# Optimization experiments

Measured on AMD Instinct MI355X. Metric: run time of the kernel, lower is better.

## Reference

```python
import jax, jax.numpy as jnp
import numpy as np

N_NODES = 50000
N_EDGES = 1600000
D_EDGE = 64
D_VERT = 64
D_IN = D_EDGE + 2 * D_VERT  # 192
D_HID = 128
D_OUT = 64


def setup_inputs() -> dict:
    key = jax.random.key(0)
    ks = jax.random.split(key, 8)
    edata = jax.random.normal(ks[0], (N_EDGES, D_EDGE), dtype=jnp.float32)
    vfeat = jax.random.normal(ks[1], (N_NODES, D_VERT), dtype=jnp.float32)
    W1 = jax.random.normal(ks[2], (D_IN, D_HID), dtype=jnp.float32) * (1.0 / np.sqrt(D_IN))
    b1 = jnp.zeros((D_HID,), dtype=jnp.float32)
    W2 = jax.random.normal(ks[3], (D_HID, D_OUT), dtype=jnp.float32) * (1.0 / np.sqrt(D_HID))
    b2 = jnp.zeros((D_OUT,), dtype=jnp.float32)
    senders = jax.random.randint(ks[4], (N_EDGES,), 0, N_NODES, dtype=jnp.int64)
    receivers = jax.random.randint(ks[5], (N_EDGES,), 0, N_NODES, dtype=jnp.int64)
    return {"edata": edata, "vfeat": vfeat, "W1": W1, "b1": b1,
            "W2": W2, "b2": b2, "senders": senders, "receivers": receivers}


def reference(edata, vfeat, W1, b1, W2, b2, senders, receivers):
    # Per-edge gather of receiver/sender vertex features, concat with edge
    # features (matches torch.cat([edata[e], v[recv], v[send]]) per edge,
    # vectorized), then updater MLP: Linear -> ReLU -> Linear.
    x = jnp.concatenate([edata, vfeat[receivers], vfeat[senders]], axis=-1)  # [E, 192]
    h = jax.nn.relu(x @ W1 + b1)  # [E, 128]
    return h @ W2 + b2            # [E, 64]
```

## Files before the change

### kernel.cpp

```cpp
#include <hip/hip_runtime.h>
#include <hip/hip_bf16.h>

#define E_TOTAL   1600000
#define NV        50000
#define DE        64
#define DV        64
#define DIN       192
#define DHID      128
#define DOUT      64
#define TILE_M    64
#define XS        200
#define HS        136
#define NTILES    (E_TOTAL / TILE_M)

typedef __bf16 bf16x8  __attribute__((ext_vector_type(8)));
typedef __bf16 bf16x4  __attribute__((ext_vector_type(4)));
typedef float  floatx4 __attribute__((ext_vector_type(4)));
typedef float  fx4     __attribute__((ext_vector_type(4)));

static __device__ __forceinline__ unsigned short f2bf(float f) {
    unsigned int u = __float_as_uint(f);
    u += 0x7fffu + ((u >> 16) & 1u);
    return (unsigned short)(u >> 16);
}

__global__ void prep_kernel(const float* __restrict__ W1, const float* __restrict__ W2,
                            const float* __restrict__ vfeat,
                            unsigned short* __restrict__ w1t,
                            unsigned short* __restrict__ w2t,
                            unsigned short* __restrict__ vfb, int do_vfb) {
    int tid = blockIdx.x * blockDim.x + threadIdx.x;
    int stride = gridDim.x * blockDim.x;
    for (int i = tid; i < DIN * DHID; i += stride) {
        int n = i / DIN, k = i % DIN;
        w1t[i] = f2bf(W1[k * DHID + n]);
    }
    for (int i = tid; i < DHID * DOUT; i += stride) {
        int n = i / DHID, k = i % DHID;
        w2t[i] = f2bf(W2[k * DOUT + n]);
    }
    if (do_vfb) {
        const fx4* src = (const fx4*)vfeat;
        ushort4* dst = (ushort4*)vfb;
        int n4 = NV * DV / 4;
        for (int i = tid; i < n4; i += stride) {
            fx4 v = src[i];
            ushort4 o;
            o.x = f2bf(v[0]); o.y = f2bf(v[1]); o.z = f2bf(v[2]); o.w = f2bf(v[3]);
            dst[i] = o;
        }
    }
}

template <bool USE_VFB>
__global__ __launch_bounds__(256, 2) void edge_mlp(
    const float* __restrict__ edata,
    const float* __restrict__ vfeat,
    const float* __restrict__ b1,
    const float* __restrict__ b2,
    const int* __restrict__ senders,
    const int* __restrict__ receivers,
    const unsigned short* __restrict__ w1t,
    const unsigned short* __restrict__ w2t,
    const unsigned short* __restrict__ vfb,
    float* __restrict__ out) {
    __shared__ unsigned short xb[TILE_M * XS];
    __shared__ unsigned short hb[TILE_M * HS];

    const int tid  = threadIdx.x;
    const int lane = tid & 63;
    const int wave = tid >> 6;
    const int l15  = lane & 15;
    const int quad = lane >> 4;

    bf16x8 w1f[6][2];
    bf16x8 w2f[4];
    {
        for (int nb = 0; nb < 2; ++nb) {
            int n = wave * 32 + nb * 16 + l15;
            const unsigned short* p = w1t + n * DIN + quad * 8;
            for (int ks = 0; ks < 6; ++ks)
                w1f[ks][nb] = *(const bf16x8*)(p + ks * 32);
        }
        int n2 = wave * 16 + l15;
        const unsigned short* p2 = w2t + n2 * DHID + quad * 8;
        for (int ks = 0; ks < 4; ++ks)
            w2f[ks] = *(const bf16x8*)(p2 + ks * 32);
    }
    float b1v[2][4], b2v[4];
#pragma unroll
    for (int nb = 0; nb < 2; ++nb)
#pragma unroll
        for (int r = 0; r < 4; ++r)
            b1v[nb][r] = b1[wave * 32 + nb * 16 + quad * 4 + r];
#pragma unroll
    for (int r = 0; r < 4; ++r)
        b2v[r] = b2[wave * 16 + quad * 4 + r];

    for (int t = blockIdx.x; t < NTILES; t += gridDim.x) {
        const long e0 = (long)t * TILE_M;

        {
#pragma unroll
            for (int it = 0; it < 4; ++it) {
                int idx = it * 256 + tid;
                int e = idx >> 4;
                int c = idx & 15;
                fx4 v = __builtin_nontemporal_load((const fx4*)(edata + (e0 + e) * DE + c * 4));
                bf16x4 o;
                o[0] = (__bf16)v[0]; o[1] = (__bf16)v[1];
                o[2] = (__bf16)v[2]; o[3] = (__bf16)v[3];
                *(bf16x4*)(xb + e * XS + c * 4) = o;
            }
            if constexpr (USE_VFB) {
#pragma unroll
                for (int it = 0; it < 4; ++it) {
                    int idx = it * 256 + tid;
                    int e = idx >> 4;
                    int g = (idx >> 3) & 1;
                    int c = idx & 7;
                    int row = g ? senders[e0 + e] : receivers[e0 + e];
                    uint4 v = *(const uint4*)(vfb + row * DV + c * 8);
                    *(uint4*)(xb + e * XS + DE + g * DV + c * 8) = v;
                }
            } else {
#pragma unroll
                for (int it = 0; it < 8; ++it) {
                    int idx = it * 256 + tid;
                    int e = idx >> 5;
                    int g = (idx >> 4) & 1;
                    int c = idx & 15;
                    int row = g ? senders[e0 + e] : receivers[e0 + e];
                    fx4 v = *(const fx4*)(vfeat + (long)row * DV + c * 4);
                    bf16x4 o;
                    o[0] = (__bf16)v[0]; o[1] = (__bf16)v[1];
                    o[2] = (__bf16)v[2]; o[3] = (__bf16)v[3];
                    *(bf16x4*)(xb + e * XS + DE + g * DV + c * 4) = o;
                }
            }
        }
        __syncthreads();

        floatx4 acc[4][2];
#pragma unroll
        for (int mb = 0; mb < 4; ++mb)
#pragma unroll
            for (int nb = 0; nb < 2; ++nb)
                acc[mb][nb] = (floatx4){b1v[nb][0], b1v[nb][1], b1v[nb][2], b1v[nb][3]};
#pragma unroll
        for (int ks = 0; ks < 6; ++ks) {
            bf16x8 a[4];
#pragma unroll
            for (int mb = 0; mb < 4; ++mb)
                a[mb] = *(const bf16x8*)(xb + (mb * 16 + l15) * XS + ks * 32 + quad * 8);
#pragma unroll
            for (int mb = 0; mb < 4; ++mb)
#pragma unroll
                for (int nb = 0; nb < 2; ++nb)
                    acc[mb][nb] = __builtin_amdgcn_mfma_f32_16x16x32_bf16(
                        w1f[ks][nb], a[mb], acc[mb][nb], 0, 0, 0);
        }

#pragma unroll
        for (int mb = 0; mb < 4; ++mb)
#pragma unroll
            for (int nb = 0; nb < 2; ++nb) {
                bf16x4 o;
#pragma unroll
                for (int r = 0; r < 4; ++r) {
                    float v = acc[mb][nb][r];
                    o[r] = (__bf16)(v > 0.f ? v : 0.f);
                }
                *(bf16x4*)(hb + (mb * 16 + l15) * HS + wave * 32 + nb * 16 + quad * 4) = o;
            }
        __syncthreads();

        floatx4 acc2[4];
#pragma unroll
        for (int mb = 0; mb < 4; ++mb)
            acc2[mb] = (floatx4){b2v[0], b2v[1], b2v[2], b2v[3]};
#pragma unroll
        for (int ks = 0; ks < 4; ++ks)
#pragma unroll
            for (int mb = 0; mb < 4; ++mb) {
                bf16x8 a2 = *(const bf16x8*)(hb + (mb * 16 + l15) * HS + ks * 32 + quad * 8);
                acc2[mb] = __builtin_amdgcn_mfma_f32_16x16x32_bf16(w2f[ks], a2, acc2[mb], 0, 0, 0);
            }

#pragma unroll
        for (int mb = 0; mb < 4; ++mb)
            *(fx4*)(out + (e0 + mb * 16 + l15) * DOUT + wave * 16 + quad * 4) = acc2[mb];
    }
}

extern "C" void kernel_launch(void* const* d_in, const int* in_sizes, int n_in,
                              void* d_out, int out_size, void* d_ws, size_t ws_size,
                              hipStream_t stream) {
    const float* edata     = (const float*)d_in[0];
    const float* vfeat     = (const float*)d_in[1];
    const float* W1        = (const float*)d_in[2];
    const float* b1        = (const float*)d_in[3];
    const float* W2        = (const float*)d_in[4];
    const float* b2        = (const float*)d_in[5];
    const int*   senders   = (const int*)d_in[6];
    const int*   receivers = (const int*)d_in[7];
    float* out = (float*)d_out;

    unsigned short* w1t = (unsigned short*)d_ws;
    unsigned short* w2t = w1t + DIN * DHID;
    unsigned short* vfb = w2t + DHID * DOUT;
    const size_t need_vfb = (size_t)(DIN * DHID + DHID * DOUT + NV * DV) * sizeof(unsigned short);
    const bool use_vfb = ws_size >= need_vfb;

    prep_kernel<<<512, 256, 0, stream>>>(W1, W2, vfeat, w1t, w2t, vfb, use_vfb ? 1 : 0);
    if (use_vfb)
        edge_mlp<true><<<1536, 256, 0, stream>>>(edata, vfeat, b1, b2, senders, receivers,
                                                 w1t, w2t, vfb, out);
    else
        edge_mlp<false><<<1536, 256, 0, stream>>>(edata, vfeat, b1, b2, senders, receivers,
                                                  w1t, w2t, vfb, out);
}
```

Before: 821.1 us.

## Repartition second GEMM by rows per wave and raise occupancy target

```diff
diff --git a/kernel.cpp b/kernel.cpp
--- a/kernel.cpp
+++ b/kernel.cpp
@@ -53,7 +53,7 @@
 }
 
 template <bool USE_VFB>
-__global__ __launch_bounds__(256, 2) void edge_mlp(
+__global__ __launch_bounds__(256, 3) void edge_mlp(
     const float* __restrict__ edata,
     const float* __restrict__ vfeat,
     const float* __restrict__ b1,
@@ -74,28 +74,30 @@
     const int quad = lane >> 4;
 
     bf16x8 w1f[6][2];
-    bf16x8 w2f[4];
+    bf16x8 w2f[4][4];
     {
+#pragma unroll
         for (int nb = 0; nb < 2; ++nb) {
-            int n = wave * 32 + nb * 16 + l15;
-            const unsigned short* p = w1t + n * DIN + quad * 8;
+            const unsigned short* p = w1t + (wave * 32 + nb * 16 + l15) * DIN + quad * 8;
+#pragma unroll
             for (int ks = 0; ks < 6; ++ks)
                 w1f[ks][nb] = *(const bf16x8*)(p + ks * 32);
         }
-        int n2 = wave * 16 + l15;
-        const unsigned short* p2 = w2t + n2 * DHID + quad * 8;
-        for (int ks = 0; ks < 4; ++ks)
-            w2f[ks] = *(const bf16x8*)(p2 + ks * 32);
-    }
-    float b1v[2][4], b2v[4];
+#pragma unroll
+        for (int nbk = 0; nbk < 4; ++nbk) {
+            const unsigned short* p2 = w2t + (nbk * 16 + l15) * DHID + quad * 8;
+#pragma unroll
+            for (int ks = 0; ks < 4; ++ks)
+                w2f[nbk][ks] = *(const bf16x8*)(p2 + ks * 32);
+        }
+    }
+    fx4 b1v[2], b2v[4];
 #pragma unroll
     for (int nb = 0; nb < 2; ++nb)
-#pragma unroll
-        for (int r = 0; r < 4; ++r)
-            b1v[nb][r] = b1[wave * 32 + nb * 16 + quad * 4 + r];
-#pragma unroll
-    for (int r = 0; r < 4; ++r)
-        b2v[r] = b2[wave * 16 + quad * 4 + r];
+        b1v[nb] = *(const fx4*)(b1 + wave * 32 + nb * 16 + quad * 4);
+#pragma unroll
+    for (int nbk = 0; nbk < 4; ++nbk)
+        b2v[nbk] = *(const fx4*)(b2 + nbk * 16 + quad * 4);
 
     for (int t = blockIdx.x; t < NTILES; t += gridDim.x) {
         const long e0 = (long)t * TILE_M;
@@ -141,55 +143,62 @@
         }
         __syncthreads();
 
-        floatx4 acc[4][2];
-#pragma unroll
-        for (int mb = 0; mb < 4; ++mb)
-#pragma unroll
-            for (int nb = 0; nb < 2; ++nb)
-                acc[mb][nb] = (floatx4){b1v[nb][0], b1v[nb][1], b1v[nb][2], b1v[nb][3]};
-#pragma unroll
-        for (int ks = 0; ks < 6; ++ks) {
-            bf16x8 a[4];
-#pragma unroll
-            for (int mb = 0; mb < 4; ++mb)
-                a[mb] = *(const bf16x8*)(xb + (mb * 16 + l15) * XS + ks * 32 + quad * 8);
-#pragma unroll
-            for (int mb = 0; mb < 4; ++mb)
+#pragma unroll
+        for (int half = 0; half < 2; ++half) {
+            floatx4 acc[2][2];
+#pragma unroll
+            for (int m = 0; m < 2; ++m)
 #pragma unroll
                 for (int nb = 0; nb < 2; ++nb)
-                    acc[mb][nb] = __builtin_amdgcn_mfma_f32_16x16x32_bf16(
-                        w1f[ks][nb], a[mb], acc[mb][nb], 0, 0, 0);
-        }
-
-#pragma unroll
-        for (int mb = 0; mb < 4; ++mb)
-#pragma unroll
-            for (int nb = 0; nb < 2; ++nb) {
-                bf16x4 o;
-#pragma unroll
-                for (int r = 0; r < 4; ++r) {
-                    float v = acc[mb][nb][r];
-                    o[r] = (__bf16)(v > 0.f ? v : 0.f);
+                    acc[m][nb] = (floatx4){b1v[nb][0], b1v[nb][1], b1v[nb][2], b1v[nb][3]};
+#pragma unroll
+            for (int ks = 0; ks < 6; ++ks) {
+                bf16x8 a[2];
+#pragma unroll
+                for (int m = 0; m < 2; ++m)
+                    a[m] = *(const bf16x8*)(xb + ((half * 2 + m) * 16 + l15) * XS + ks * 32 + quad * 8);
+#pragma unroll
+                for (int m = 0; m < 2; ++m)
+#pragma unroll
+                    for (int nb = 0; nb < 2; ++nb)
+                        acc[m][nb] = __builtin_amdgcn_mfma_f32_16x16x32_bf16(
+                            w1f[ks][nb], a[m], acc[m][nb], 0, 0, 0);
+            }
+#pragma unroll
+            for (int m = 0; m < 2; ++m)
+#pragma unroll
+                for (int nb = 0; nb < 2; ++nb) {
+                    bf16x4 o;
+#pragma unroll
+                    for (int r = 0; r < 4; ++r) {
+                        float v = acc[m][nb][r];
+                        o[r] = (__bf16)(v > 0.f ? v : 0.f);
+                    }
+                    *(bf16x4*)(hb + ((half * 2 + m) * 16 + l15) * HS
+                               + wave * 32 + nb * 16 + quad * 4) = o;
                 }
-                *(bf16x4*)(hb + (mb * 16 + l15) * HS + wave * 32 + nb * 16 + quad * 4) = o;
-            }
+        }
         __syncthreads();
 
         floatx4 acc2[4];
 #pragma unroll
-        for (int mb = 0; mb < 4; ++mb)
-            acc2[mb] = (floatx4){b2v[0], b2v[1], b2v[2], b2v[3]};
-#pragma unroll
-        for (int ks = 0; ks < 4; ++ks)
-#pragma unroll
-            for (int mb = 0; mb < 4; ++mb) {
-                bf16x8 a2 = *(const bf16x8*)(hb + (mb * 16 + l15) * HS + ks * 32 + quad * 8);
-                acc2[mb] = __builtin_amdgcn_mfma_f32_16x16x32_bf16(w2f[ks], a2, acc2[mb], 0, 0, 0);
-            }
-
-#pragma unroll
-        for (int mb = 0; mb < 4; ++mb)
-            *(fx4*)(out + (e0 + mb * 16 + l15) * DOUT + wave * 16 + quad * 4) = acc2[mb];
+        for (int nbk = 0; nbk < 4; ++nbk)
+            acc2[nbk] = (floatx4){b2v[nbk][0], b2v[nbk][1], b2v[nbk][2], b2v[nbk][3]};
+#pragma unroll
+        for (int ks = 0; ks < 4; ++ks) {
+            bf16x8 a2 = *(const bf16x8*)(hb + (wave * 16 + l15) * HS + ks * 32 + quad * 8);
+#pragma unroll
+            for (int nbk = 0; nbk < 4; ++nbk)
+                acc2[nbk] = __builtin_amdgcn_mfma_f32_16x16x32_bf16(
+                    w2f[nbk][ks], a2, acc2[nbk], 0, 0, 0);
+        }
+
+#pragma unroll
+        for (int nbk = 0; nbk < 4; ++nbk)
+            __builtin_nontemporal_store(acc2[nbk],
+                (fx4*)(out + (e0 + wave * 16 + l15) * DOUT + nbk * 16 + quad * 4));
+
+        __syncthreads();
     }
 }
 
```

Result: slower. 848.1 us (+3.3%).
